# Performance work log

Hardware: AMD Instinct MI355X
Metric: run time of the kernel (lower is better)

The kernel has to match this reference:

```python
import jax, jax.numpy as jnp
import numpy as np

D_MODEL = 1024
NUM_HEADS = 16
HEAD_DIM = D_MODEL // NUM_HEADS


def setup_inputs() -> dict:
    key = jax.random.key(0)
    ks = jax.random.split(key, 5)
    x = jax.random.normal(ks[0], (2, 2048, D_MODEL), dtype=jnp.float32)
    # torch nn.Linear init scale ~ U(-1/sqrt(in), 1/sqrt(in)); use small normals
    s = 1.0 / np.sqrt(D_MODEL)
    W_qkv = jax.random.normal(ks[1], (D_MODEL, 3 * D_MODEL), dtype=jnp.float32) * s
    b_qkv = jax.random.normal(ks[2], (3 * D_MODEL,), dtype=jnp.float32) * s
    W_out = jax.random.normal(ks[3], (D_MODEL, D_MODEL), dtype=jnp.float32) * s
    b_out = jax.random.normal(ks[4], (D_MODEL,), dtype=jnp.float32) * s
    return {"x": x, "W_qkv": W_qkv, "b_qkv": b_qkv, "W_out": W_out, "b_out": b_out}


def reference(x, W_qkv, b_qkv, W_out, b_out):
    B, S, _ = x.shape
    qkv = x @ W_qkv + b_qkv                                  # [B,S,3D]
    qkv = qkv.reshape(B, S, NUM_HEADS, 3 * HEAD_DIM).transpose(0, 2, 1, 3)  # [B,H,S,3d]
    q, k, v = jnp.split(qkv, 3, axis=-1)                     # each [B,H,S,d]
    scale = 1.0 / np.sqrt(HEAD_DIM)
    scores = jnp.einsum("bhqd,bhkd->bhqk", q, k) * scale      # [B,H,S,S]
    attn = jax.nn.softmax(scores, axis=-1)
    values = jnp.einsum("bhqk,bhkd->bhqd", attn, v)           # [B,H,S,d]
    values = values.transpose(0, 2, 1, 3).reshape(B, S, D_MODEL)
    return values @ W_out + b_out
```

## Files before the change

kernel.cpp:

```cpp
#include <hip/hip_runtime.h>


#define D_MODEL 1024
#define NHEAD   16
#define HDIM    64
#define SEQ     2048
#define BATCH   2
#define NTOK    (BATCH * SEQ)

typedef float    f32x4 __attribute__((ext_vector_type(4)));
typedef _Float16 f16x8 __attribute__((ext_vector_type(8)));
typedef _Float16 f16x4 __attribute__((ext_vector_type(4)));

#define GLOBAL_LOAD_LDS16(gptr, lptr)                                            \
    __builtin_amdgcn_global_load_lds(                                            \
        (const __attribute__((address_space(1))) unsigned int*)(gptr),           \
        (__attribute__((address_space(3))) unsigned int*)(lptr), 16, 0, 0)

__global__ __launch_bounds__(256) void convert_x_kernel(
    const float* __restrict__ x, _Float16* __restrict__ xh, int n)
{
    const int i = (blockIdx.x * 256 + threadIdx.x) * 4;
    if (i >= n) return;
    const float4 v = *(const float4*)&x[i];
    f16x4 h;
    h[0] = (_Float16)v.x; h[1] = (_Float16)v.y;
    h[2] = (_Float16)v.z; h[3] = (_Float16)v.w;
    *(f16x4*)&xh[i] = h;
}

__global__ __launch_bounds__(256) void transpose_w_kernel(
    const float* __restrict__ W, _Float16* __restrict__ Wt, int K, int N)
{
    __shared__ float ts[64][65];
    const int tid = threadIdx.x;
    const int n0 = blockIdx.x * 64, k0 = blockIdx.y * 64;
    {
        const int r = tid >> 2;
        const int c = (tid & 3) << 4;
        const float* src = W + (size_t)(k0 + r) * N + n0 + c;
        #pragma unroll
        for (int u = 0; u < 4; ++u)
            *(float4*)&ts[r][c + u * 4] = *(const float4*)&src[u * 4];
    }
    __syncthreads();
    {
        const int n = tid >> 2;
        const int kg = (tid & 3) << 4;
        f16x8 v0, v1;
        #pragma unroll
        for (int j = 0; j < 8; ++j) {
            v0[j] = (_Float16)ts[kg + j][n];
            v1[j] = (_Float16)ts[kg + 8 + j][n];
        }
        _Float16* dst = Wt + (size_t)(n0 + n) * K + k0 + kg;
        *(f16x8*)&dst[0] = v0;
        *(f16x8*)&dst[8] = v1;
    }
}

template<int OUT_F16>
__global__ __launch_bounds__(256) void gemm_f16_kernel(
    const _Float16* __restrict__ A, const _Float16* __restrict__ Bt,
    const float* __restrict__ bias, void* __restrict__ Cout,
    int M, int N, int K)
{
    __shared__ _Float16 lds[2][4096];
    const int tid = threadIdx.x;
    const int wave = tid >> 6, lane = tid & 63;
    const int quad = lane >> 4, l16 = lane & 15;
    const int m0 = blockIdx.y * 128, n0 = blockIdx.x * 128;
    const int wr = wave >> 1, wc = wave & 1;

    f32x4 acc[4][4] = {};

    const _Float16* gsrc = (wave < 2) ? (A + (size_t)m0 * K) : (Bt + (size_t)n0 * K);
    _Float16* ldst = (wave < 2) ? &lds[0][0] : &lds[1][0];
    const int sbase = (wave & 1) * 4;

    for (int k0 = 0; k0 < K; k0 += 32) {
        __syncthreads();
        #pragma unroll
        for (int j = 0; j < 4; ++j) {
            const int seg = sbase + j;
            const int chunk = seg >> 1;
            const int row = ((seg & 1) << 6) | lane;
            GLOBAL_LOAD_LDS16(gsrc + (size_t)row * K + k0 + chunk * 8, ldst + seg * 512);
        }
        __syncthreads();

        f16x8 a[4], b[4];
        #pragma unroll
        for (int mt = 0; mt < 4; ++mt)
            a[mt] = *(const f16x8*)&lds[0][quad * 1024 + (wr * 64 + mt * 16 + l16) * 8];
        #pragma unroll
        for (int nt = 0; nt < 4; ++nt)
            b[nt] = *(const f16x8*)&lds[1][quad * 1024 + (wc * 64 + nt * 16 + l16) * 8];
        #pragma unroll
        for (int mt = 0; mt < 4; ++mt)
            #pragma unroll
            for (int nt = 0; nt < 4; ++nt)
                acc[mt][nt] = __builtin_amdgcn_mfma_f32_16x16x32_f16(a[mt], b[nt], acc[mt][nt], 0, 0, 0);
    }

    #pragma unroll
    for (int nt = 0; nt < 4; ++nt) {
        const int col = n0 + wc * 64 + nt * 16 + l16;
        const float bv = bias[col];
        #pragma unroll
        for (int mt = 0; mt < 4; ++mt) {
            #pragma unroll
            for (int r = 0; r < 4; ++r) {
                const int row = m0 + wr * 64 + mt * 16 + quad * 4 + r;
                const float v = acc[mt][nt][r] + bv;
                if (OUT_F16) ((_Float16*)Cout)[(size_t)row * N + col] = (_Float16)v;
                else         ((float*)Cout)[(size_t)row * N + col] = v;
            }
        }
    }
}

__global__ __launch_bounds__(256) void swizzle_kv_kernel(
    const _Float16* __restrict__ qkv,
    _Float16* __restrict__ Ksw, _Float16* __restrict__ Vsw)
{
    __shared__ _Float16 ts[64][72];
    const int tid = threadIdx.x;
    const int s0 = blockIdx.x * 64, h = blockIdx.y, b = blockIdx.z;
    const size_t hsz = (size_t)8 * SEQ * 8;
    _Float16* kh = Ksw + (size_t)(b * NHEAD + h) * hsz;
    _Float16* vh = Vsw + (size_t)(b * NHEAD + h) * hsz;

    {
        const int s = s0 + (tid >> 2);
        const int dg = (tid & 3) << 4;
        const _Float16* src = qkv + (size_t)(b * SEQ + s) * (3 * D_MODEL) + h * (3 * HDIM) + HDIM + dg;
        const f16x8 v0 = *(const f16x8*)&src[0];
        const f16x8 v1 = *(const f16x8*)&src[8];
        const int c0 = dg >> 3;
        *(f16x8*)&kh[((size_t)c0 * SEQ + s) * 8]       = v0;
        *(f16x8*)&kh[((size_t)(c0 + 1) * SEQ + s) * 8] = v1;
    }

    {
        const int s = tid >> 2, dg = (tid & 3) << 4;
        const _Float16* src = qkv + (size_t)(b * SEQ + s0 + s) * (3 * D_MODEL) + h * (3 * HDIM) + 2 * HDIM + dg;
        *(f16x8*)&ts[s][dg]     = *(const f16x8*)&src[0];
        *(f16x8*)&ts[s][dg + 8] = *(const f16x8*)&src[8];
    }
    __syncthreads();
    {
        const int d = tid >> 2, sg = (tid & 3) << 4;
        f16x8 v0, v1;
        #pragma unroll
        for (int j = 0; j < 8; ++j) { v0[j] = ts[sg + j][d]; v1[j] = ts[sg + 8 + j][d]; }
        const int cs0 = (s0 + sg) >> 3;
        *(f16x8*)&vh[((size_t)cs0 * HDIM + d) * 8]       = v0;
        *(f16x8*)&vh[((size_t)(cs0 + 1) * HDIM + d) * 8] = v1;
    }
}

__global__ __launch_bounds__(256) void attn_mfma_kernel(
    const _Float16* __restrict__ qkv,
    const _Float16* __restrict__ Ksw, const _Float16* __restrict__ Vsw,
    _Float16* __restrict__ val)
{
    __shared__ _Float16 Ks[8 * 64 * 8];
    __shared__ _Float16 Vts[8 * 64 * 8];
    __shared__ _Float16 Ps[64 * 72];

    const int tid = threadIdx.x;
    const int wave = tid >> 6, lane = tid & 63;
    const int quad = lane >> 4, l16 = lane & 15;
    const int qt = blockIdx.x, h = blockIdx.y, b = blockIdx.z;
    const int q0 = qt * 64;

    const size_t hsz = (size_t)8 * SEQ * 8;
    const _Float16* kh = Ksw + (size_t)(b * NHEAD + h) * hsz;
    const _Float16* vh = Vsw + (size_t)(b * NHEAD + h) * hsz;

    f16x8 qf[2];
    {
        const int row = q0 + wave * 16 + l16;
        const _Float16* src = qkv + (size_t)(b * SEQ + row) * (3 * D_MODEL) + h * (3 * HDIM) + quad * 8;
        const f16x8 t0 = *(const f16x8*)(src);
        const f16x8 t1 = *(const f16x8*)(src + 32);
        #pragma unroll
        for (int j = 0; j < 8; ++j) {
            qf[0][j] = (_Float16)((float)t0[j] * 0.1803368802f);
            qf[1][j] = (_Float16)((float)t1[j] * 0.1803368802f);
        }
    }

    f32x4 acc[4] = {};
    float rs = 0.f;

    for (int kt = 0; kt < SEQ / 64; ++kt) {
        __syncthreads();
        #pragma unroll
        for (int jj = 0; jj < 2; ++jj) {
            const int c = wave * 2 + jj;
            GLOBAL_LOAD_LDS16(kh + ((size_t)c * SEQ + kt * 64 + lane) * 8, Ks + c * 512);
            GLOBAL_LOAD_LDS16(vh + ((size_t)(kt * 8 + c) * HDIM + lane) * 8, Vts + c * 512);
        }
        __syncthreads();

        f32x4 s[4] = {};
        #pragma unroll
        for (int mt = 0; mt < 4; ++mt) {
            const f16x8 kA0 = *(const f16x8*)&Ks[quad * 512 + (mt * 16 + l16) * 8];
            const f16x8 kA1 = *(const f16x8*)&Ks[(4 + quad) * 512 + (mt * 16 + l16) * 8];
            s[mt] = __builtin_amdgcn_mfma_f32_16x16x32_f16(kA0, qf[0], s[mt], 0, 0, 0);
            s[mt] = __builtin_amdgcn_mfma_f32_16x16x32_f16(kA1, qf[1], s[mt], 0, 0, 0);
        }

        #pragma unroll
        for (int mt = 0; mt < 4; ++mt) {
            const float p0 = __builtin_amdgcn_exp2f(s[mt][0]);
            const float p1 = __builtin_amdgcn_exp2f(s[mt][1]);
            const float p2 = __builtin_amdgcn_exp2f(s[mt][2]);
            const float p3 = __builtin_amdgcn_exp2f(s[mt][3]);
            rs += (p0 + p1) + (p2 + p3);
            uint2 w;
            w.x = __builtin_bit_cast(unsigned, __builtin_amdgcn_cvt_pkrtz(p0, p1));
            w.y = __builtin_bit_cast(unsigned, __builtin_amdgcn_cvt_pkrtz(p2, p3));
            *(uint2*)&Ps[(wave * 16 + l16) * 72 + mt * 16 + quad * 4] = w;
        }

        const f16x8 pA0 = *(const f16x8*)&Ps[(wave * 16 + l16) * 72 + quad * 8];
        const f16x8 pA1 = *(const f16x8*)&Ps[(wave * 16 + l16) * 72 + 32 + quad * 8];
        #pragma unroll
        for (int nt = 0; nt < 4; ++nt) {
            const f16x8 v0 = *(const f16x8*)&Vts[quad * 512 + (nt * 16 + l16) * 8];
            const f16x8 v1 = *(const f16x8*)&Vts[(4 + quad) * 512 + (nt * 16 + l16) * 8];
            acc[nt] = __builtin_amdgcn_mfma_f32_16x16x32_f16(pA0, v0, acc[nt], 0, 0, 0);
            acc[nt] = __builtin_amdgcn_mfma_f32_16x16x32_f16(pA1, v1, acc[nt], 0, 0, 0);
        }
    }

    rs += __shfl_xor(rs, 16);
    rs += __shfl_xor(rs, 32);
    const float inv = 1.f / rs;
    float invr[4];
    #pragma unroll
    for (int r = 0; r < 4; ++r)
        invr[r] = __shfl(inv, quad * 4 + r, 16);

    #pragma unroll
    for (int r = 0; r < 4; ++r) {
        const int row = b * SEQ + q0 + wave * 16 + quad * 4 + r;
        #pragma unroll
        for (int nt = 0; nt < 4; ++nt) {
            const int col = h * HDIM + nt * 16 + l16;
            val[(size_t)row * D_MODEL + col] = (_Float16)(acc[nt][r] * invr[r]);
        }
    }
}

extern "C" void kernel_launch(void* const* d_in, const int* in_sizes, int n_in,
                              void* d_out, int out_size, void* d_ws, size_t ws_size,
                              hipStream_t stream)
{
    const float* x     = (const float*)d_in[0];
    const float* W_qkv = (const float*)d_in[1];
    const float* b_qkv = (const float*)d_in[2];
    const float* W_out = (const float*)d_in[3];
    const float* b_out = (const float*)d_in[4];

    char* ws = (char*)d_ws;
    _Float16* Ksw   = (_Float16*)ws;
    _Float16* val_h = (_Float16*)(ws + (8u << 20));
    _Float16* wq_t  = (_Float16*)(ws + (16u << 20));
    _Float16* wo_t  = (_Float16*)(ws + (22u << 20));
    _Float16* qkv_h = (_Float16*)(ws + (24u << 20));
    _Float16* x_h   = (_Float16*)(ws + (48u << 20));
    _Float16* Vsw   = (_Float16*)(ws + (48u << 20));

    convert_x_kernel<<<NTOK * D_MODEL / 1024, 256, 0, stream>>>(x, x_h, NTOK * D_MODEL);
    transpose_w_kernel<<<dim3(3 * D_MODEL / 64, D_MODEL / 64), 256, 0, stream>>>(
        W_qkv, wq_t, D_MODEL, 3 * D_MODEL);
    gemm_f16_kernel<1><<<dim3(3 * D_MODEL / 128, NTOK / 128), 256, 0, stream>>>(
        x_h, wq_t, b_qkv, qkv_h, NTOK, 3 * D_MODEL, D_MODEL);
    swizzle_kv_kernel<<<dim3(SEQ / 64, NHEAD, BATCH), 256, 0, stream>>>(qkv_h, Ksw, Vsw);
    attn_mfma_kernel<<<dim3(SEQ / 64, NHEAD, BATCH), 256, 0, stream>>>(qkv_h, Ksw, Vsw, val_h);
    transpose_w_kernel<<<dim3(D_MODEL / 64, D_MODEL / 64), 256, 0, stream>>>(
        W_out, wo_t, D_MODEL, D_MODEL);
    gemm_f16_kernel<0><<<dim3(D_MODEL / 128, NTOK / 128), 256, 0, stream>>>(
        val_h, wo_t, b_out, d_out, NTOK, D_MODEL, D_MODEL);
}
```

Measured before the change: 245.5 us.

## Fuse prep kernels into one launch and double GEMM K-tile to 64

Merges the x conversion and both weight transposes into a single prep kernel dispatched by block index, removing two kernel launches. The f16 GEMM now stages a 64-wide K slice per iteration instead of 32, halving the number of synchronisation barriers and global-to-LDS rounds per tile. LDS use per block doubles to 32KB, which may reduce occupancy.

Result: no change. 247.7 us (+0.9%).

```diff
diff --git a/kernel.cpp b/kernel.cpp
--- a/kernel.cpp
+++ b/kernel.cpp
@@ -17,27 +17,35 @@
         (const __attribute__((address_space(1))) unsigned int*)(gptr),           \
         (__attribute__((address_space(3))) unsigned int*)(lptr), 16, 0, 0)
 
-__global__ __launch_bounds__(256) void convert_x_kernel(
-    const float* __restrict__ x, _Float16* __restrict__ xh, int n)
-{
-    const int i = (blockIdx.x * 256 + threadIdx.x) * 4;
-    if (i >= n) return;
-    const float4 v = *(const float4*)&x[i];
-    f16x4 h;
-    h[0] = (_Float16)v.x; h[1] = (_Float16)v.y;
-    h[2] = (_Float16)v.z; h[3] = (_Float16)v.w;
-    *(f16x4*)&xh[i] = h;
-}
-
-__global__ __launch_bounds__(256) void transpose_w_kernel(
-    const float* __restrict__ W, _Float16* __restrict__ Wt, int K, int N)
-{
+__global__ __launch_bounds__(256) void prep_kernel(
+    const float* __restrict__ x, _Float16* __restrict__ xh,
+    const float* __restrict__ Wqkv, _Float16* __restrict__ wq_t,
+    const float* __restrict__ Wout, _Float16* __restrict__ wo_t)
+{
+    const int bx = blockIdx.x;
+    const int tid = threadIdx.x;
+    if (bx < 4096) {
+        const int i = (bx * 256 + tid) * 4;
+        const float4 v = *(const float4*)&x[i];
+        f16x4 hh;
+        hh[0] = (_Float16)v.x; hh[1] = (_Float16)v.y;
+        hh[2] = (_Float16)v.z; hh[3] = (_Float16)v.w;
+        *(f16x4*)&xh[i] = hh;
+        return;
+    }
     __shared__ float ts[64][65];
-    const int tid = threadIdx.x;
-    const int n0 = blockIdx.x * 64, k0 = blockIdx.y * 64;
-    {
-        const int r = tid >> 2;
-        const int c = (tid & 3) << 4;
+    const float* W; _Float16* Wt; int N, n0, k0;
+    if (bx < 4096 + 768) {
+        const int local = bx - 4096;
+        W = Wqkv; Wt = wq_t; N = 3072;
+        n0 = (local % 48) * 64; k0 = (local / 48) * 64;
+    } else {
+        const int local = bx - 4864;
+        W = Wout; Wt = wo_t; N = 1024;
+        n0 = (local % 16) * 64; k0 = (local / 16) * 64;
+    }
+    {
+        const int r = tid >> 2, c = (tid & 3) << 4;
         const float* src = W + (size_t)(k0 + r) * N + n0 + c;
         #pragma unroll
         for (int u = 0; u < 4; ++u)
@@ -45,15 +53,14 @@
     }
     __syncthreads();
     {
-        const int n = tid >> 2;
-        const int kg = (tid & 3) << 4;
+        const int n = tid >> 2, kg = (tid & 3) << 4;
         f16x8 v0, v1;
         #pragma unroll
         for (int j = 0; j < 8; ++j) {
             v0[j] = (_Float16)ts[kg + j][n];
             v1[j] = (_Float16)ts[kg + 8 + j][n];
         }
-        _Float16* dst = Wt + (size_t)(n0 + n) * K + k0 + kg;
+        _Float16* dst = Wt + (size_t)(n0 + n) * D_MODEL + k0 + kg;
         *(f16x8*)&dst[0] = v0;
         *(f16x8*)&dst[8] = v1;
     }
@@ -65,7 +72,7 @@
     const float* __restrict__ bias, void* __restrict__ Cout,
     int M, int N, int K)
 {
-    __shared__ _Float16 lds[2][4096];
+    __shared__ _Float16 lds[2][8192];
     const int tid = threadIdx.x;
     const int wave = tid >> 6, lane = tid & 63;
     const int quad = lane >> 4, l16 = lane & 15;
@@ -76,12 +83,12 @@
 
     const _Float16* gsrc = (wave < 2) ? (A + (size_t)m0 * K) : (Bt + (size_t)n0 * K);
     _Float16* ldst = (wave < 2) ? &lds[0][0] : &lds[1][0];
-    const int sbase = (wave & 1) * 4;
-
-    for (int k0 = 0; k0 < K; k0 += 32) {
-        __syncthreads();
-        #pragma unroll
-        for (int j = 0; j < 4; ++j) {
+    const int sbase = (wave & 1) * 8;
+
+    for (int k0 = 0; k0 < K; k0 += 64) {
+        __syncthreads();
+        #pragma unroll
+        for (int j = 0; j < 8; ++j) {
             const int seg = sbase + j;
             const int chunk = seg >> 1;
             const int row = ((seg & 1) << 6) | lane;
@@ -89,18 +96,21 @@
         }
         __syncthreads();
 
-        f16x8 a[4], b[4];
-        #pragma unroll
-        for (int mt = 0; mt < 4; ++mt)
-            a[mt] = *(const f16x8*)&lds[0][quad * 1024 + (wr * 64 + mt * 16 + l16) * 8];
-        #pragma unroll
-        for (int nt = 0; nt < 4; ++nt)
-            b[nt] = *(const f16x8*)&lds[1][quad * 1024 + (wc * 64 + nt * 16 + l16) * 8];
-        #pragma unroll
-        for (int mt = 0; mt < 4; ++mt)
+        #pragma unroll
+        for (int kk = 0; kk < 2; ++kk) {
+            f16x8 a[4], b[4];
+            #pragma unroll
+            for (int mt = 0; mt < 4; ++mt)
+                a[mt] = *(const f16x8*)&lds[0][(kk * 4 + quad) * 1024 + (wr * 64 + mt * 16 + l16) * 8];
             #pragma unroll
             for (int nt = 0; nt < 4; ++nt)
-                acc[mt][nt] = __builtin_amdgcn_mfma_f32_16x16x32_f16(a[mt], b[nt], acc[mt][nt], 0, 0, 0);
+                b[nt] = *(const f16x8*)&lds[1][(kk * 4 + quad) * 1024 + (wc * 64 + nt * 16 + l16) * 8];
+            #pragma unroll
+            for (int mt = 0; mt < 4; ++mt)
+                #pragma unroll
+                for (int nt = 0; nt < 4; ++nt)
+                    acc[mt][nt] = __builtin_amdgcn_mfma_f32_16x16x32_f16(a[mt], b[nt], acc[mt][nt], 0, 0, 0);
+        }
     }
 
     #pragma unroll
@@ -141,7 +151,6 @@
         *(f16x8*)&kh[((size_t)c0 * SEQ + s) * 8]       = v0;
         *(f16x8*)&kh[((size_t)(c0 + 1) * SEQ + s) * 8] = v1;
     }
-
     {
         const int s = tid >> 2, dg = (tid & 3) << 4;
         const _Float16* src = qkv + (size_t)(b * SEQ + s0 + s) * (3 * D_MODEL) + h * (3 * HDIM) + 2 * HDIM + dg;
@@ -276,15 +285,11 @@
     _Float16* x_h   = (_Float16*)(ws + (48u << 20));
     _Float16* Vsw   = (_Float16*)(ws + (48u << 20));
 
-    convert_x_kernel<<<NTOK * D_MODEL / 1024, 256, 0, stream>>>(x, x_h, NTOK * D_MODEL);
-    transpose_w_kernel<<<dim3(3 * D_MODEL / 64, D_MODEL / 64), 256, 0, stream>>>(
-        W_qkv, wq_t, D_MODEL, 3 * D_MODEL);
+    prep_kernel<<<5120, 256, 0, stream>>>(x, x_h, W_qkv, wq_t, W_out, wo_t);
     gemm_f16_kernel<1><<<dim3(3 * D_MODEL / 128, NTOK / 128), 256, 0, stream>>>(
         x_h, wq_t, b_qkv, qkv_h, NTOK, 3 * D_MODEL, D_MODEL);
     swizzle_kv_kernel<<<dim3(SEQ / 64, NHEAD, BATCH), 256, 0, stream>>>(qkv_h, Ksw, Vsw);
     attn_mfma_kernel<<<dim3(SEQ / 64, NHEAD, BATCH), 256, 0, stream>>>(qkv_h, Ksw, Vsw, val_h);
-    transpose_w_kernel<<<dim3(D_MODEL / 64, D_MODEL / 64), 256, 0, stream>>>(
-        W_out, wo_t, D_MODEL, D_MODEL);
     gemm_f16_kernel<0><<<dim3(D_MODEL / 128, NTOK / 128), 256, 0, stream>>>(
         val_h, wo_t, b_out, d_out, NTOK, D_MODEL, D_MODEL);
 }
```
